# Kernel optimization log

Hardware: AMD Instinct MI355X
Metric: run time of the kernel (lower is better)

Reference implementation:

```python
import jax, jax.numpy as jnp
import numpy as np
import math

IN_CH = 512
OUT_CH = 512
K = 3
STYLE_DIM = 512
B, H, W = 8, 64, 64


def setup_inputs() -> dict:
    key = jax.random.key(0)
    k1, k2, k3, k4 = jax.random.split(key, 4)
    return {
        "input": jax.random.normal(k1, (B, IN_CH, H, W), dtype=jnp.float32),
        "style": jax.random.normal(k2, (B, STYLE_DIM), dtype=jnp.float32),
        "weight": jax.random.normal(k3, (1, OUT_CH, IN_CH, K, K), dtype=jnp.float32),
        "mod_weight": jax.random.normal(k4, (IN_CH, STYLE_DIM), dtype=jnp.float32),
        "mod_bias": jnp.ones((IN_CH,), dtype=jnp.float32),
    }


def reference(input, style, weight, mod_weight, mod_bias):
    batch, in_ch, h, w = input.shape
    out_ch = weight.shape[1]
    k = weight.shape[-1]
    conv_scale = 1.0 / math.sqrt(in_ch * k * k)
    lin_scale = 1.0 / math.sqrt(STYLE_DIM)  # EqualLinear scale, lr_mul=1

    # modulation: EqualLinear(style_dim -> in_channel), bias_init=1, no activation
    s = style @ (mod_weight * lin_scale).T + mod_bias  # [B, Cin]

    # per-sample modulated weight: [B, Cout, Cin, K, K]
    wmod = conv_scale * weight * s[:, None, :, None, None]
    demod = jax.lax.rsqrt(jnp.sum(wmod * wmod, axis=(2, 3, 4)) + 1e-8)  # [B, Cout]
    wmod = wmod * demod[:, :, None, None, None]

    # grouped conv with groups = batch (exactly mirrors the torch path)
    lhs = input.reshape(1, batch * in_ch, h, w)
    rhs = wmod.reshape(batch * out_ch, in_ch, k, k)
    pad = (k - 1) // 2
    out = jax.lax.conv_general_dilated(
        lhs, rhs,
        window_strides=(1, 1),
        padding=[(pad, pad), (pad, pad)],
        dimension_numbers=("NCHW", "OIHW", "NCHW"),
        feature_group_count=batch,
    )
    return out.reshape(batch, out_ch, h, w)
```

## Files before the change

kernel.cpp:

```cpp
#include <hip/hip_runtime.h>
#include <hip/hip_bf16.h>
#include <stdint.h>

typedef __attribute__((ext_vector_type(8))) short bf16x8;
typedef __attribute__((ext_vector_type(4))) float f32x4;
typedef __attribute__((ext_vector_type(8))) unsigned short u16x8;

__device__ __forceinline__ unsigned short f2bf(float f) {
  unsigned int u = __float_as_uint(f);
  u = u + 0x7fffu + ((u >> 16) & 1u);
  return (unsigned short)(u >> 16);
}

__global__ void k_sw(const float* __restrict__ style, const float* __restrict__ mw,
                     const float* __restrict__ mb, const float* __restrict__ w,
                     float* __restrict__ s, float* __restrict__ wsq) {
  if (blockIdx.x < 8) {
    __shared__ float st[512];
    const int b = blockIdx.x, t = threadIdx.x;
    st[t]       = style[b*512 + t];
    st[t + 256] = style[b*512 + t + 256];
    __syncthreads();
    for (int k = 0; k < 2; ++k) {
      int c = t + k*256;
      const float* row = mw + (size_t)c * 512;
      float acc = 0.f;
      for (int j = 0; j < 512; ++j) acc += st[j] * row[j];
      s[b*512 + c] = acc * 0.04419417382415922f + mb[c];
    }
  } else {
    int g = (blockIdx.x - 8) * 256 + threadIdx.x;
    const float* p = w + (size_t)g * 9;
    float acc = 0.f;
    #pragma unroll
    for (int t = 0; t < 9; ++t) { float v = p[t]; acc += v*v; }
    wsq[g] = acc;
  }
}

__global__ void k_demod(const float* __restrict__ s, const float* __restrict__ wsq,
                        float* __restrict__ dm) {
  __shared__ float s2[512];
  const int g = blockIdx.x * 256 + threadIdx.x;
  const int b = g >> 9, o = g & 511, t = threadIdx.x;
  float v0 = s[b*512 + t], v1 = s[b*512 + t + 256];
  s2[t] = v0*v0; s2[t+256] = v1*v1;
  __syncthreads();
  const float* row = wsq + (size_t)o * 512;
  float acc = 0.f;
  for (int j = 0; j < 512; ++j) acc += s2[j] * row[j];
  dm[g] = rsqrtf(acc * (1.0f/4608.0f) + 1e-8f);
}

__global__ void k_wt(const float* __restrict__ w, float* __restrict__ wt) {
  const int id = blockIdx.x * 256 + threadIdx.x;
  const int c8 = id & 7, o = (id >> 3) & 511, cb = (id >> 12) & 7, kk = id >> 15;
  const int ci0 = cb*64 + c8*8;
  float v[8];
  #pragma unroll
  for (int e = 0; e < 8; ++e) v[e] = w[((size_t)(o*512 + ci0 + e))*9 + kk];
  float* dst = wt + (((size_t)(kk*8 + cb)*512 + o)*64 + c8*8);
  *(f32x4*)dst       = (f32x4){v[0],v[1],v[2],v[3]};
  *(f32x4*)(dst + 4) = (f32x4){v[4],v[5],v[6],v[7]};
}

__global__ void k_wprep2(const float* __restrict__ wt, const float* __restrict__ s,
                         const float* __restrict__ dm, unsigned short* __restrict__ wp) {
  const int id = blockIdx.x * 256 + threadIdx.x;
  const int b = blockIdx.y;
  const int c8 = id & 7, o = (id >> 3) & 511, cb = (id >> 12) & 7, kk = id >> 15;
  const int ci0 = cb*64 + c8*8;
  const float dmo = 0.014731391274719739f  * dm[b*512 + o];
  f32x4 s0 = *(const f32x4*)(s + b*512 + ci0);
  f32x4 s1 = *(const f32x4*)(s + b*512 + ci0 + 4);
  const float* src = wt + (((size_t)(kk*8 + cb)*512 + o)*64 + c8*8);
  f32x4 w0 = *(const f32x4*)src, w1 = *(const f32x4*)(src + 4);
  u16x8 h;
  #pragma unroll
  for (int e = 0; e < 4; ++e) h[e]     = f2bf(w0[e] * s0[e] * dmo);
  #pragma unroll
  for (int e = 0; e < 4; ++e) h[e + 4] = f2bf(w1[e] * s1[e] * dmo);
  char* base = (char*)wp + ((((size_t)b*9 + kk)*8 + cb)*512 + o)*128
             + ((unsigned)(c8*16) ^ (unsigned)((o & 7) << 4));
  *(u16x8*)base = h;
}

__global__ __launch_bounds__(512, 2) void k_conv(const float* __restrict__ in,
                                                 const unsigned short* __restrict__ wp,
                                                 float* __restrict__ out) {
  __shared__ __align__(16) unsigned char ldsA[3*32768];
  __shared__ __align__(16) unsigned char ldsB[49152];

  const int tid = threadIdx.x;
  const int lan15 = tid & 15;
  const int lgrp = (tid >> 4) & 3;
  const int wid = tid >> 6;
  const int wm = wid >> 2, wn = wid & 3;
  const unsigned wg = blockIdx.x;
  const int b = wg & 7, pt = (wg >> 3) & 15, ot = (wg >> 7) & 1;
  const int o0 = ot * 256, y0 = pt * 4;

  const float* inb = in + (size_t)b * 512 * 4096;
  const unsigned short* wpb = wp + (size_t)b * 9 * 8 * 512 * 64;

  auto stageA = [&](int tap, int cbb, int buf) {
    const char* src = (const char*)(wpb + (((size_t)tap*8 + cbb)*512 + (size_t)o0) * 64);
    unsigned char* dst = ldsA + buf*32768;
    #pragma unroll
    for (int r = 0; r < 4; ++r) {
      __builtin_amdgcn_global_load_lds(
        (const __attribute__((address_space(1))) unsigned int*)(src + tid*16 + r*8192),
        (__attribute__((address_space(3))) unsigned int*)(dst + tid*16 + r*8192),
        16, 0, 0);
    }
  };

  f32x4 bv0[6], bv1[6];
  unsigned bp[6][4];
  auto loadB = [&](int cbb) {
    const int cp = tid & 31, xq = (tid >> 5) & 15;
    #pragma unroll
    for (int j = 0; j < 6; ++j) {
      const int yi = y0 - 1 + j;
      const int yc = yi < 0 ? 0 : (yi > 63 ? 63 : yi);
      const float* p0 = inb + ((size_t)(cbb*64 + cp*2) * 64 + yc) * 64 + xq*4;
      bv0[j] = *(const f32x4*)p0;
      bv1[j] = *(const f32x4*)(p0 + 4096);
    }
  };
  auto convB = [&]() {
    #pragma unroll
    for (int j = 0; j < 6; ++j)
      #pragma unroll
      for (int e = 0; e < 4; ++e)
        bp[j][e] = (unsigned)f2bf(bv0[j][e]) | ((unsigned)f2bf(bv1[j][e]) << 16);
  };
  auto writeB = [&]() {
    const int cp = tid & 31, xq = (tid >> 5) & 15;
    #pragma unroll
    for (int j = 0; j < 6; ++j) {
      const int yi = y0 - 1 + j;
      const bool valid = (yi >= 0) & (yi < 64);
      #pragma unroll
      for (int e = 0; e < 4; ++e) {
        const int x = xq*4 + e;
        *(unsigned*)(ldsB + j*8192 + x*128 + ((cp*4) ^ ((x & 7) << 4))) = valid ? bp[j][e] : 0u;
      }
    }
  };

  f32x4 acc[8][4];
  #pragma unroll
  for (int mf = 0; mf < 8; ++mf)
    #pragma unroll
    for (int nf = 0; nf < 4; ++nf)
      acc[mf][nf] = (f32x4){0.f, 0.f, 0.f, 0.f};

  const int aB0 = (wm*128 + lan15)*128 + ((lgrp*16) ^ ((lan15 & 7) << 4));
  const int aB1 = aB0 ^ 64;
  int cB0[3], cB1[3];
  #pragma unroll
  for (int kx = 0; kx < 3; ++kx) {
    const int x0 = lan15 + kx - 1;
    cB0[kx] = wn*8192 + x0*128 + ((lgrp*16) ^ ((x0 & 7) << 4));
    cB1[kx] = cB0[kx] ^ 64;
  }
  const bool zL = (lan15 == 0), zR = (lan15 == 15);

#define BARR asm volatile("s_barrier" ::: "memory")
#define GATE(N) asm volatile("s_waitcnt vmcnt(" #N ")\n\ts_barrier" ::: "memory")

#define RD_A(MH, KS) _Pragma("unroll") \
    for (int i = 0; i < 4; ++i) \
      af[i] = *(const bf16x8*)(Ab + ((KS) ? aB1 : aB0) + ((MH)*4 + i)*2048);

#define RD_B(KS) _Pragma("unroll") \
    for (int nf = 0; nf < 4; ++nf) { \
      bf16x8 v = *(const bf16x8*)(Bb + ((KS) ? cB1[kx_] : cB0[kx_]) + nf*2048); \
      if (kx_ == 0 && nf == 0) { if (zL) v = (bf16x8){0,0,0,0,0,0,0,0}; } \
      if (kx_ == 2 && nf == 3) { if (zR) v = (bf16x8){0,0,0,0,0,0,0,0}; } \
      bfr[nf] = v; }

#define MF16(MH) { __builtin_amdgcn_s_setprio(1); \
    _Pragma("unroll") for (int i = 0; i < 4; ++i) \
      _Pragma("unroll") for (int nf = 0; nf < 4; ++nf) \
        acc[(MH)*4+i][nf] = __builtin_amdgcn_mfma_f32_16x16x32_bf16(af[i], bfr[nf], acc[(MH)*4+i][nf], 0, 0, 0); \
    __builtin_amdgcn_s_setprio(0); }

#define PH4 \
    RD_A(0,0) RD_B(0) MF16(0) \
    RD_A(1,0) BARR; MF16(1) \
    RD_A(0,1) RD_B(1) BARR; MF16(0) \
    RD_A(1,1) BARR; MF16(1)

#define TAP(KK) { \
    constexpr int ky_ = (KK)/3, kx_ = (KK)%3; \
    const unsigned char* Ab = ldsA + ((KK)%3)*32768; \
    const unsigned char* Bb = ldsB + ky_*8192 + wn*8192 - wn*8192 + (wn)*0 + (wn + 0)*0 + (wn)*0 + ky_*0; \
    (void)ky_; \
    bf16x8 af[4], bfr[4]; \
    stageA((KK)+2, cb, ((KK)+2)%3); \
    GATE(8); \
    PH4 }

#undef TAP
#define TAP(KK) { \
    constexpr int ky_ = (KK)/3, kx_ = (KK)%3; \
    const unsigned char* Ab = ldsA + ((KK)%3)*32768; \
    const unsigned char* Bb = ldsB + ky_*8192; \
    bf16x8 af[4], bfr[4]; \
    stageA((KK)+2, cb, ((KK)+2)%3); \
    GATE(8); \
    PH4 }

  loadB(0);
  asm volatile("" ::: "memory");
  stageA(0, 0, 0);
  stageA(1, 0, 1);
  asm volatile("s_waitcnt vmcnt(8)" ::: "memory");
  convB();
  writeB();
  asm volatile("s_waitcnt vmcnt(4) lgkmcnt(0)\n\ts_barrier" ::: "memory");

  for (int cb = 0; cb < 7; ++cb) {
    TAP(0) TAP(1) TAP(2) TAP(3) TAP(4) TAP(5) TAP(6)
    {
      constexpr int ky_ = 2, kx_ = 1;
      const unsigned char* Ab = ldsA + (7%3)*32768;
      const unsigned char* Bb = ldsB + ky_*8192;
      bf16x8 af[4], bfr[4];
      stageA(0, cb + 1, 0);
      GATE(8);
      loadB(cb + 1);
      PH4
    }
    {
      asm volatile("s_waitcnt vmcnt(0)" ::: "memory");
      convB();
      stageA(1, cb + 1, 1);
      constexpr int ky_ = 2, kx_ = 2;
      const unsigned char* Ab = ldsA + (8%3)*32768;
      const unsigned char* Bb = ldsB + ky_*8192;
      bf16x8 af[4], bfr[4];
      PH4
      BARR;
      writeB();
      asm volatile("s_waitcnt lgkmcnt(0)\n\ts_barrier" ::: "memory");
    }
  }
  {
    const int cb = 7;
    TAP(0) TAP(1) TAP(2) TAP(3) TAP(4) TAP(5) TAP(6)
    {
      constexpr int ky_ = 2, kx_ = 1;
      const unsigned char* Ab = ldsA + (7%3)*32768;
      const unsigned char* Bb = ldsB + ky_*8192;
      bf16x8 af[4], bfr[4];
      GATE(4);
      PH4
    }
    {
      asm volatile("s_waitcnt vmcnt(0)" ::: "memory");
      constexpr int ky_ = 2, kx_ = 2;
      const unsigned char* Ab = ldsA + (8%3)*32768;
      const unsigned char* Bb = ldsB + ky_*8192;
      bf16x8 af[4], bfr[4];
      PH4
    }
  }

  float* outb = out + (size_t)b * 512 * 4096;
  #pragma unroll
  for (int mf = 0; mf < 8; ++mf) {
    const int o = o0 + wm*128 + mf*16 + lgrp*4;
    #pragma unroll
    for (int nf = 0; nf < 4; ++nf) {
      const int p = pt*256 + wn*64 + nf*16 + lan15;
      #pragma unroll
      for (int r = 0; r < 4; ++r)
        outb[(size_t)(o + r) * 4096 + p] = acc[mf][nf][r];
    }
  }
#undef TAP
#undef PH4
#undef MF16
#undef RD_B
#undef RD_A
#undef GATE
#undef BARR
}

extern "C" void kernel_launch(void* const* d_in, const int* in_sizes, int n_in,
                              void* d_out, int out_size, void* d_ws, size_t ws_size,
                              hipStream_t stream) {
  const float* input  = (const float*)d_in[0];
  const float* style  = (const float*)d_in[1];
  const float* weight = (const float*)d_in[2];
  const float* mw     = (const float*)d_in[3];
  const float* mb     = (const float*)d_in[4];
  float* out = (float*)d_out;
  char* ws = (char*)d_ws;
  float* s     = (float*)ws;
  float* demod = (float*)(ws + 16384);
  float* wsq   = (float*)(ws + 32768);
  float* wt    = (float*)(ws + 1081344);
  unsigned short* wp = (unsigned short*)(ws + 10518528);

  hipLaunchKernelGGL(k_wt,     dim3(1152),     dim3(256), 0, stream, weight, wt);
  hipLaunchKernelGGL(k_sw,     dim3(1032),     dim3(256), 0, stream, style, mw, mb, weight, s, wsq);
  hipLaunchKernelGGL(k_demod,  dim3(16),       dim3(256), 0, stream, s, wsq, demod);
  hipLaunchKernelGGL(k_wprep2, dim3(1152, 8),  dim3(256), 0, stream, wt, s, demod, wp);
  hipLaunchKernelGGL(k_conv,   dim3(256),      dim3(512), 0, stream, input, wp, out);
}
```

Before: 197.5 us.

## Merge weight-transpose and style kernels; restructure conv tap pipeline with earlier B prefetch

Folds the weight-transpose kernel into the style/wsq kernel, so one fewer launch is needed. In the conv main loop, the next channel block's input load (loadB) is issued two taps earlier, and its convert/write is moved after the last tap, giving deeper vmcnt gating. Each MFMA group is now fenced by barriers, lgkmcnt waits and sched_barriers, to pin the interleave of LDS reads and MFMAs. The extra barriers add sync overhead and could serialize waves more than before.

```diff
diff --git a/kernel.cpp b/kernel.cpp
--- a/kernel.cpp
+++ b/kernel.cpp
@@ -12,12 +12,23 @@
   return (unsigned short)(u >> 16);
 }
 
-__global__ void k_sw(const float* __restrict__ style, const float* __restrict__ mw,
-                     const float* __restrict__ mb, const float* __restrict__ w,
-                     float* __restrict__ s, float* __restrict__ wsq) {
-  if (blockIdx.x < 8) {
+__global__ void k1(const float* __restrict__ w, const float* __restrict__ style,
+                   const float* __restrict__ mw, const float* __restrict__ mb,
+                   float* __restrict__ wt, float* __restrict__ s, float* __restrict__ wsq) {
+  const int bid = blockIdx.x, t = threadIdx.x;
+  if (bid < 1152) {
+    const int id = bid * 256 + t;
+    const int c8 = id & 7, o = (id >> 3) & 511, cb = (id >> 12) & 7, kk = id >> 15;
+    const int ci0 = cb*64 + c8*8;
+    float v[8];
+    #pragma unroll
+    for (int e = 0; e < 8; ++e) v[e] = w[((size_t)(o*512 + ci0 + e))*9 + kk];
+    float* dst = wt + (((size_t)(kk*8 + cb)*512 + o)*64 + c8*8);
+    *(f32x4*)dst       = (f32x4){v[0],v[1],v[2],v[3]};
+    *(f32x4*)(dst + 4) = (f32x4){v[4],v[5],v[6],v[7]};
+  } else if (bid < 1160) {
     __shared__ float st[512];
-    const int b = blockIdx.x, t = threadIdx.x;
+    const int b = bid - 1152;
     st[t]       = style[b*512 + t];
     st[t + 256] = style[b*512 + t + 256];
     __syncthreads();
@@ -29,11 +40,11 @@
       s[b*512 + c] = acc * 0.04419417382415922f + mb[c];
     }
   } else {
-    int g = (blockIdx.x - 8) * 256 + threadIdx.x;
+    int g = (bid - 1160) * 256 + t;
     const float* p = w + (size_t)g * 9;
     float acc = 0.f;
     #pragma unroll
-    for (int t = 0; t < 9; ++t) { float v = p[t]; acc += v*v; }
+    for (int q = 0; q < 9; ++q) { float v = p[q]; acc += v*v; }
     wsq[g] = acc;
   }
 }
@@ -52,18 +63,6 @@
   dm[g] = rsqrtf(acc * (1.0f/4608.0f) + 1e-8f);
 }
 
-__global__ void k_wt(const float* __restrict__ w, float* __restrict__ wt) {
-  const int id = blockIdx.x * 256 + threadIdx.x;
-  const int c8 = id & 7, o = (id >> 3) & 511, cb = (id >> 12) & 7, kk = id >> 15;
-  const int ci0 = cb*64 + c8*8;
-  float v[8];
-  #pragma unroll
-  for (int e = 0; e < 8; ++e) v[e] = w[((size_t)(o*512 + ci0 + e))*9 + kk];
-  float* dst = wt + (((size_t)(kk*8 + cb)*512 + o)*64 + c8*8);
-  *(f32x4*)dst       = (f32x4){v[0],v[1],v[2],v[3]};
-  *(f32x4*)(dst + 4) = (f32x4){v[4],v[5],v[6],v[7]};
-}
-
 __global__ void k_wprep2(const float* __restrict__ wt, const float* __restrict__ s,
                          const float* __restrict__ dm, unsigned short* __restrict__ wp) {
   const int id = blockIdx.x * 256 + threadIdx.x;
@@ -169,6 +168,8 @@
 
 #define BARR asm volatile("s_barrier" ::: "memory")
 #define GATE(N) asm volatile("s_waitcnt vmcnt(" #N ")\n\ts_barrier" ::: "memory")
+#define WK0 asm volatile("s_waitcnt lgkmcnt(0)" ::: "memory"); __builtin_amdgcn_sched_barrier(0);
+#define PIN asm volatile("" ::: "memory")
 
 #define RD_A(MH, KS) _Pragma("unroll") \
     for (int i = 0; i < 4; ++i) \
@@ -185,25 +186,18 @@
     _Pragma("unroll") for (int i = 0; i < 4; ++i) \
       _Pragma("unroll") for (int nf = 0; nf < 4; ++nf) \
         acc[(MH)*4+i][nf] = __builtin_amdgcn_mfma_f32_16x16x32_bf16(af[i], bfr[nf], acc[(MH)*4+i][nf], 0, 0, 0); \
-    __builtin_amdgcn_s_setprio(0); }
-
-#define PH4 \
-    RD_A(0,0) RD_B(0) MF16(0) \
-    RD_A(1,0) BARR; MF16(1) \
-    RD_A(0,1) RD_B(1) BARR; MF16(0) \
-    RD_A(1,1) BARR; MF16(1)
-
-#define TAP(KK) { \
-    constexpr int ky_ = (KK)/3, kx_ = (KK)%3; \
-    const unsigned char* Ab = ldsA + ((KK)%3)*32768; \
-    const unsigned char* Bb = ldsB + ky_*8192 + wn*8192 - wn*8192 + (wn)*0 + (wn + 0)*0 + (wn)*0 + ky_*0; \
-    (void)ky_; \
-    bf16x8 af[4], bfr[4]; \
-    stageA((KK)+2, cb, ((KK)+2)%3); \
-    GATE(8); \
-    PH4 }
-
-#undef TAP
+    __builtin_amdgcn_s_setprio(0); __builtin_amdgcn_sched_barrier(0); }
+
+#define TAPBODY \
+    RD_A(0,0) RD_B(0) \
+    BARR; WK0 MF16(0) BARR; \
+    RD_A(1,0) \
+    BARR; WK0 MF16(1) BARR; \
+    RD_A(0,1) RD_B(1) \
+    BARR; WK0 MF16(0) BARR; \
+    RD_A(1,1) \
+    BARR; WK0 MF16(1)
+
 #define TAP(KK) { \
     constexpr int ky_ = (KK)/3, kx_ = (KK)%3; \
     const unsigned char* Ab = ldsA + ((KK)%3)*32768; \
@@ -211,61 +205,81 @@
     bf16x8 af[4], bfr[4]; \
     stageA((KK)+2, cb, ((KK)+2)%3); \
     GATE(8); \
-    PH4 }
+    TAPBODY }
 
   loadB(0);
-  asm volatile("" ::: "memory");
+  PIN;
   stageA(0, 0, 0);
   stageA(1, 0, 1);
   asm volatile("s_waitcnt vmcnt(8)" ::: "memory");
   convB();
   writeB();
-  asm volatile("s_waitcnt vmcnt(4) lgkmcnt(0)\n\ts_barrier" ::: "memory");
+  asm volatile("s_waitcnt lgkmcnt(0)\n\ts_barrier" ::: "memory");
 
   for (int cb = 0; cb < 7; ++cb) {
-    TAP(0) TAP(1) TAP(2) TAP(3) TAP(4) TAP(5) TAP(6)
+    TAP(0) TAP(1) TAP(2) TAP(3) TAP(4) TAP(5)
+    {
+      constexpr int ky_ = 2, kx_ = 0;
+      const unsigned char* Ab = ldsA + (6%3)*32768;
+      const unsigned char* Bb = ldsB + ky_*8192;
+      bf16x8 af[4], bfr[4];
+      stageA(8, cb, 2);
+      PIN;
+      loadB(cb + 1);
+      GATE(20);
+      TAPBODY
+    }
     {
       constexpr int ky_ = 2, kx_ = 1;
       const unsigned char* Ab = ldsA + (7%3)*32768;
       const unsigned char* Bb = ldsB + ky_*8192;
       bf16x8 af[4], bfr[4];
       stageA(0, cb + 1, 0);
-      GATE(8);
-      loadB(cb + 1);
-      PH4
-    }
-    {
-      asm volatile("s_waitcnt vmcnt(0)" ::: "memory");
-      convB();
-      stageA(1, cb + 1, 1);
+      GATE(20);
+      TAPBODY
+    }
+    {
       constexpr int ky_ = 2, kx_ = 2;
       const unsigned char* Ab = ldsA + (8%3)*32768;
       const unsigned char* Bb = ldsB + ky_*8192;
       bf16x8 af[4], bfr[4];
-      PH4
-      BARR;
-      writeB();
-      asm volatile("s_waitcnt lgkmcnt(0)\n\ts_barrier" ::: "memory");
-    }
+      stageA(1, cb + 1, 1);
+      GATE(20);
+      TAPBODY
+    }
+    asm volatile("s_waitcnt vmcnt(8)" ::: "memory");
+    convB();
+    BARR;
+    writeB();
+    asm volatile("s_waitcnt lgkmcnt(0)\n\ts_barrier" ::: "memory");
   }
   {
     const int cb = 7;
-    TAP(0) TAP(1) TAP(2) TAP(3) TAP(4) TAP(5) TAP(6)
+    TAP(0) TAP(1) TAP(2) TAP(3) TAP(4) TAP(5)
+    {
+      constexpr int ky_ = 2, kx_ = 0;
+      const unsigned char* Ab = ldsA + (6%3)*32768;
+      const unsigned char* Bb = ldsB + ky_*8192;
+      bf16x8 af[4], bfr[4];
+      stageA(8, 7, 2);
+      GATE(8);
+      TAPBODY
+    }
     {
       constexpr int ky_ = 2, kx_ = 1;
       const unsigned char* Ab = ldsA + (7%3)*32768;
       const unsigned char* Bb = ldsB + ky_*8192;
       bf16x8 af[4], bfr[4];
       GATE(4);
-      PH4
-    }
-    {
-      asm volatile("s_waitcnt vmcnt(0)" ::: "memory");
+      TAPBODY
+    }
+    {
       constexpr int ky_ = 2, kx_ = 2;
       const unsigned char* Ab = ldsA + (8%3)*32768;
       const unsigned char* Bb = ldsB + ky_*8192;
       bf16x8 af[4], bfr[4];
-      PH4
+      GATE(0);
+      TAPBODY
     }
   }
 
@@ -282,12 +296,14 @@
     }
   }
 #undef TAP
-#undef PH4
+#undef TAPBODY
 #undef MF16
 #undef RD_B
 #undef RD_A
+#undef WK0
 #undef GATE
 #undef BARR
+#undef PIN
 }
 
 extern "C" void kernel_launch(void* const* d_in, const int* in_sizes, int n_in,
@@ -306,9 +322,8 @@
   float* wt    = (float*)(ws + 1081344);
   unsigned short* wp = (unsigned short*)(ws + 10518528);
 
-  hipLaunchKernelGGL(k_wt,     dim3(1152),     dim3(256), 0, stream, weight, wt);
-  hipLaunchKernelGGL(k_sw,     dim3(1032),     dim3(256), 0, stream, style, mw, mb, weight, s, wsq);
-  hipLaunchKernelGGL(k_demod,  dim3(16),       dim3(256), 0, stream, s, wsq, demod);
-  hipLaunchKernelGGL(k_wprep2, dim3(1152, 8),  dim3(256), 0, stream, wt, s, demod, wp);
-  hipLaunchKernelGGL(k_conv,   dim3(256),      dim3(512), 0, stream, input, wp, out);
-}
+  hipLaunchKernelGGL(k1,      dim3(2184),     dim3(256), 0, stream, weight, style, mw, mb, wt, s, wsq);
+  hipLaunchKernelGGL(k_demod, dim3(16),       dim3(256), 0, stream, s, wsq, demod);
+  hipLaunchKernelGGL(k_wprep2, dim3(1152, 8), dim3(256), 0, stream, wt, s, demod, wp);
+  hipLaunchKernelGGL(k_conv,  dim3(256),      dim3(512), 0, stream, input, wp, out);
+}
```

Measured after the change: 204.9 us. 3.7% more time.

## Fold style modulation into input and demod into epilogue, share one bf16 weight

Applied to the files above, without the earlier changes.

Instead of building a per-batch modulated bf16 weight tensor (8 copies), the weight is converted to bf16 once and shared across batches. The style scale is applied to input activations during the fp32->bf16 conversion in the conv's B-load path, and the demodulation factor (with conv scale folded in) is applied per output channel in the store epilogue. This removes the large per-batch weight prep kernel and the transposed fp32 intermediate, merges prep kernels into one launch, and cuts launch count from five to three. It changes rounding slightly, since the product is quantized differently, and adds a few multiplies to the conv kernel.

```diff
diff --git a/kernel.cpp b/kernel.cpp
--- a/kernel.cpp
+++ b/kernel.cpp
@@ -12,12 +12,24 @@
   return (unsigned short)(u >> 16);
 }
 
-__global__ void k_sw(const float* __restrict__ style, const float* __restrict__ mw,
-                     const float* __restrict__ mb, const float* __restrict__ w,
-                     float* __restrict__ s, float* __restrict__ wsq) {
-  if (blockIdx.x < 8) {
+__global__ void k1(const float* __restrict__ w, const float* __restrict__ style,
+                   const float* __restrict__ mw, const float* __restrict__ mb,
+                   unsigned short* __restrict__ wp, float* __restrict__ s,
+                   float* __restrict__ wsq) {
+  const int bid = blockIdx.x, t = threadIdx.x;
+  if (bid < 1152) {
+    const int id = bid * 256 + t;
+    const int c8 = id & 7, o = (id >> 3) & 511, cb = (id >> 12) & 7, kk = id >> 15;
+    const int ci0 = cb*64 + c8*8;
+    u16x8 h;
+    #pragma unroll
+    for (int e = 0; e < 8; ++e) h[e] = f2bf(w[((size_t)(o*512 + ci0 + e))*9 + kk]);
+    char* base = (char*)wp + (((size_t)kk*8 + cb)*512 + o)*128
+               + ((unsigned)(c8*16) ^ (unsigned)((o & 7) << 4));
+    *(u16x8*)base = h;
+  } else if (bid < 1160) {
     __shared__ float st[512];
-    const int b = blockIdx.x, t = threadIdx.x;
+    const int b = bid - 1152;
     st[t]       = style[b*512 + t];
     st[t + 256] = style[b*512 + t + 256];
     __syncthreads();
@@ -29,11 +41,11 @@
       s[b*512 + c] = acc * 0.04419417382415922f + mb[c];
     }
   } else {
-    int g = (blockIdx.x - 8) * 256 + threadIdx.x;
+    int g = (bid - 1160) * 256 + t;
     const float* p = w + (size_t)g * 9;
     float acc = 0.f;
     #pragma unroll
-    for (int t = 0; t < 9; ++t) { float v = p[t]; acc += v*v; }
+    for (int q = 0; q < 9; ++q) { float v = p[q]; acc += v*v; }
     wsq[g] = acc;
   }
 }
@@ -49,44 +61,13 @@
   const float* row = wsq + (size_t)o * 512;
   float acc = 0.f;
   for (int j = 0; j < 512; ++j) acc += s2[j] * row[j];
-  dm[g] = rsqrtf(acc * (1.0f/4608.0f) + 1e-8f);
-}
-
-__global__ void k_wt(const float* __restrict__ w, float* __restrict__ wt) {
-  const int id = blockIdx.x * 256 + threadIdx.x;
-  const int c8 = id & 7, o = (id >> 3) & 511, cb = (id >> 12) & 7, kk = id >> 15;
-  const int ci0 = cb*64 + c8*8;
-  float v[8];
-  #pragma unroll
-  for (int e = 0; e < 8; ++e) v[e] = w[((size_t)(o*512 + ci0 + e))*9 + kk];
-  float* dst = wt + (((size_t)(kk*8 + cb)*512 + o)*64 + c8*8);
-  *(f32x4*)dst       = (f32x4){v[0],v[1],v[2],v[3]};
-  *(f32x4*)(dst + 4) = (f32x4){v[4],v[5],v[6],v[7]};
-}
-
-__global__ void k_wprep2(const float* __restrict__ wt, const float* __restrict__ s,
-                         const float* __restrict__ dm, unsigned short* __restrict__ wp) {
-  const int id = blockIdx.x * 256 + threadIdx.x;
-  const int b = blockIdx.y;
-  const int c8 = id & 7, o = (id >> 3) & 511, cb = (id >> 12) & 7, kk = id >> 15;
-  const int ci0 = cb*64 + c8*8;
-  const float dmo = 0.014731391274719739f  * dm[b*512 + o];
-  f32x4 s0 = *(const f32x4*)(s + b*512 + ci0);
-  f32x4 s1 = *(const f32x4*)(s + b*512 + ci0 + 4);
-  const float* src = wt + (((size_t)(kk*8 + cb)*512 + o)*64 + c8*8);
-  f32x4 w0 = *(const f32x4*)src, w1 = *(const f32x4*)(src + 4);
-  u16x8 h;
-  #pragma unroll
-  for (int e = 0; e < 4; ++e) h[e]     = f2bf(w0[e] * s0[e] * dmo);
-  #pragma unroll
-  for (int e = 0; e < 4; ++e) h[e + 4] = f2bf(w1[e] * s1[e] * dmo);
-  char* base = (char*)wp + ((((size_t)b*9 + kk)*8 + cb)*512 + o)*128
-             + ((unsigned)(c8*16) ^ (unsigned)((o & 7) << 4));
-  *(u16x8*)base = h;
+  dm[g] = 0.014731391274719739f * rsqrtf(acc * (1.0f/4608.0f) + 1e-8f);
 }
 
 __global__ __launch_bounds__(512, 2) void k_conv(const float* __restrict__ in,
                                                  const unsigned short* __restrict__ wp,
+                                                 const float* __restrict__ s,
+                                                 const float* __restrict__ dm,
                                                  float* __restrict__ out) {
   __shared__ __align__(16) unsigned char ldsA[3*32768];
   __shared__ __align__(16) unsigned char ldsB[49152];
@@ -101,10 +82,9 @@
   const int o0 = ot * 256, y0 = pt * 4;
 
   const float* inb = in + (size_t)b * 512 * 4096;
-  const unsigned short* wpb = wp + (size_t)b * 9 * 8 * 512 * 64;
 
   auto stageA = [&](int tap, int cbb, int buf) {
-    const char* src = (const char*)(wpb + (((size_t)tap*8 + cbb)*512 + (size_t)o0) * 64);
+    const char* src = (const char*)(wp + (((size_t)tap*8 + cbb)*512 + (size_t)o0) * 64);
     unsigned char* dst = ldsA + buf*32768;
     #pragma unroll
     for (int r = 0; r < 4; ++r) {
@@ -116,24 +96,28 @@
   };
 
   f32x4 bv0[6], bv1[6];
+  float sv0, sv1;
   unsigned bp[6][4];
   auto loadB = [&](int cbb) {
     const int cp = tid & 31, xq = (tid >> 5) & 15;
+    const int ci0 = cbb*64 + cp*2;
     #pragma unroll
     for (int j = 0; j < 6; ++j) {
       const int yi = y0 - 1 + j;
       const int yc = yi < 0 ? 0 : (yi > 63 ? 63 : yi);
-      const float* p0 = inb + ((size_t)(cbb*64 + cp*2) * 64 + yc) * 64 + xq*4;
+      const float* p0 = inb + ((size_t)ci0 * 64 + yc) * 64 + xq*4;
       bv0[j] = *(const f32x4*)p0;
       bv1[j] = *(const f32x4*)(p0 + 4096);
     }
+    sv0 = s[b*512 + ci0];
+    sv1 = s[b*512 + ci0 + 1];
   };
   auto convB = [&]() {
     #pragma unroll
     for (int j = 0; j < 6; ++j)
       #pragma unroll
       for (int e = 0; e < 4; ++e)
-        bp[j][e] = (unsigned)f2bf(bv0[j][e]) | ((unsigned)f2bf(bv1[j][e]) << 16);
+        bp[j][e] = (unsigned)f2bf(bv0[j][e] * sv0) | ((unsigned)f2bf(bv1[j][e] * sv1) << 16);
   };
   auto writeB = [&]() {
     const int cp = tid & 31, xq = (tid >> 5) & 15;
@@ -196,17 +180,6 @@
 #define TAP(KK) { \
     constexpr int ky_ = (KK)/3, kx_ = (KK)%3; \
     const unsigned char* Ab = ldsA + ((KK)%3)*32768; \
-    const unsigned char* Bb = ldsB + ky_*8192 + wn*8192 - wn*8192 + (wn)*0 + (wn + 0)*0 + (wn)*0 + ky_*0; \
-    (void)ky_; \
-    bf16x8 af[4], bfr[4]; \
-    stageA((KK)+2, cb, ((KK)+2)%3); \
-    GATE(8); \
-    PH4 }
-
-#undef TAP
-#define TAP(KK) { \
-    constexpr int ky_ = (KK)/3, kx_ = (KK)%3; \
-    const unsigned char* Ab = ldsA + ((KK)%3)*32768; \
     const unsigned char* Bb = ldsB + ky_*8192; \
     bf16x8 af[4], bfr[4]; \
     stageA((KK)+2, cb, ((KK)+2)%3); \
@@ -269,16 +242,18 @@
     }
   }
 
+  const float* dmb = dm + b*512;
   float* outb = out + (size_t)b * 512 * 4096;
   #pragma unroll
   for (int mf = 0; mf < 8; ++mf) {
     const int o = o0 + wm*128 + mf*16 + lgrp*4;
+    const f32x4 d4 = *(const f32x4*)(dmb + o);
     #pragma unroll
     for (int nf = 0; nf < 4; ++nf) {
       const int p = pt*256 + wn*64 + nf*16 + lan15;
       #pragma unroll
       for (int r = 0; r < 4; ++r)
-        outb[(size_t)(o + r) * 4096 + p] = acc[mf][nf][r];
+        outb[(size_t)(o + r) * 4096 + p] = acc[mf][nf][r] * d4[r];
     }
   }
 #undef TAP
@@ -301,14 +276,11 @@
   float* out = (float*)d_out;
   char* ws = (char*)d_ws;
   float* s     = (float*)ws;
-  float* demod = (float*)(ws + 16384);
+  float* dm    = (float*)(ws + 16384);
   float* wsq   = (float*)(ws + 32768);
-  float* wt    = (float*)(ws + 1081344);
-  unsigned short* wp = (unsigned short*)(ws + 10518528);
-
-  hipLaunchKernelGGL(k_wt,     dim3(1152),     dim3(256), 0, stream, weight, wt);
-  hipLaunchKernelGGL(k_sw,     dim3(1032),     dim3(256), 0, stream, style, mw, mb, weight, s, wsq);
-  hipLaunchKernelGGL(k_demod,  dim3(16),       dim3(256), 0, stream, s, wsq, demod);
-  hipLaunchKernelGGL(k_wprep2, dim3(1152, 8),  dim3(256), 0, stream, wt, s, demod, wp);
-  hipLaunchKernelGGL(k_conv,   dim3(256),      dim3(512), 0, stream, input, wp, out);
-}
+  unsigned short* wp = (unsigned short*)(ws + 1081344);
+
+  hipLaunchKernelGGL(k1,      dim3(2184), dim3(256), 0, stream, weight, style, mw, mb, wp, s, wsq);
+  hipLaunchKernelGGL(k_demod, dim3(16),   dim3(256), 0, stream, s, wsq, dm);
+  hipLaunchKernelGGL(k_conv,  dim3(256),  dim3(512), 0, stream, input, wp, s, dm, out);
+}
```

Measured after the change: 202.4 us. 2.5% more time.
